# Kernel optimization log

Measured on AMD Instinct MI355X. Metric: run time of the kernel, lower is better.

## Reference

```python
import jax, jax.numpy as jnp
import numpy as np

B, LI, LT = 1, 2048, 256
HID, HEADS, HD = 3072, 24, 128
MLP = 4 * HID  # 12288
EPS = 1e-6


def setup_inputs() -> dict:
    key = jax.random.key(0)
    ks = jax.random.split(key, 12)
    n = lambda k, s, sc=1.0: jax.random.normal(k, s, dtype=jnp.float32) * sc
    # RoPE tables, interleaved-pair layout over head_dim
    theta = 10000.0 ** (-jnp.arange(0, HD, 2, dtype=jnp.float32) / HD)  # [HD/2]
    ang = jnp.arange(LI, dtype=jnp.float32)[:, None] * theta[None, :]   # [LI, HD/2]
    freqs_cos = jnp.repeat(jnp.cos(ang), 2, axis=-1)  # [LI, HD]
    freqs_sin = jnp.repeat(jnp.sin(ang), 2, axis=-1)
    return {
        "img": n(ks[0], (B, LI, HID)),
        "txt": n(ks[1], (B, LT, HID)),
        "vec": n(ks[2], (B, HID)),
        "freqs_cos": freqs_cos,
        "freqs_sin": freqs_sin,
        "w1": n(ks[3], (3 * HID + MLP, HID), 0.02),
        "b1": jnp.zeros((3 * HID + MLP,), jnp.float32),
        "w2": n(ks[4], (HID, HID + MLP), 0.02),
        "b2": jnp.zeros((HID,), jnp.float32),
        "q_norm_w": jnp.ones((HD,), jnp.float32),
        "k_norm_w": jnp.ones((HD,), jnp.float32),
        "mod_w": n(ks[5], (3 * HID, HID), 0.02),
        "mod_b": jnp.zeros((3 * HID,), jnp.float32),
        "txt_len": LT,
    }


def _layernorm(x):  # no affine, eps=1e-6
    mu = x.mean(-1, keepdims=True)
    var = ((x - mu) ** 2).mean(-1, keepdims=True)
    return (x - mu) * jax.lax.rsqrt(var + EPS)


def _rmsnorm(x, w):  # per-head-dim RMSNorm with affine weight
    ms = (x * x).mean(-1, keepdims=True)
    return x * jax.lax.rsqrt(ms + EPS) * w


def _rope(x, cos, sin):  # x: [B,L,H,D]; interleaved complex rotation
    xr = x.reshape(*x.shape[:-1], HD // 2, 2)
    rot = jnp.stack([-xr[..., 1], xr[..., 0]], axis=-1).reshape(x.shape)
    return x * cos[None, :, None, :] + rot * sin[None, :, None, :]


def reference(img, txt, vec, freqs_cos, freqs_sin, w1, b1, w2, b2,
              q_norm_w, k_norm_w, mod_w, mod_b, txt_len):
    H = img.shape[-1]
    Li = img.shape[1]
    # modulation: SiLU(vec) @ W -> shift, scale, gate
    mod = jax.nn.silu(vec) @ mod_w.T + mod_b           # [B, 3H]
    shift, scale, gate = jnp.split(mod, 3, axis=-1)
    modulate = lambda x: x * (1.0 + scale[:, None, :]) + shift[:, None, :]
    img_mod = modulate(_layernorm(img))
    txt_mod = modulate(_layernorm(txt))
    x_mod = jnp.concatenate([img_mod, txt_mod], axis=1)  # [B,S,H]
    Bb, S = x_mod.shape[0], x_mod.shape[1]
    # fused QKV projection (slices of linear1)
    qkv = x_mod @ w1[: 3 * H].T + b1[: 3 * H]
    q, k, v = [t.reshape(Bb, S, HEADS, HD) for t in jnp.split(qkv, 3, axis=-1)]
    q = _rmsnorm(q, q_norm_w)
    k = _rmsnorm(k, k_norm_w)
    # RoPE only on the img portion of the sequence
    q = jnp.concatenate([_rope(q[:, :Li], freqs_cos, freqs_sin), q[:, Li:]], axis=1)
    k = jnp.concatenate([_rope(k[:, :Li], freqs_cos, freqs_sin), k[:, Li:]], axis=1)
    # full (non-causal) attention over img+txt tokens
    logits = jnp.einsum('bqhd,bkhd->bhqk', q, k) * (HD ** -0.5)
    probs = jax.nn.softmax(logits, axis=-1)
    attn = jnp.einsum('bhqk,bkhd->bqhd', probs, v).reshape(Bb, S, H)
    # MLP branch (linear1 mlp slice) with gelu-tanh, then fused linear2
    mlp = jax.nn.gelu(x_mod @ w1[3 * H:].T + b1[3 * H:], approximate=True)
    out = jnp.concatenate([attn, mlp], axis=-1) @ w2.T + b2  # [B,S,H]
    img_out = img + gate[:, None, :] * out[:, :-txt_len]
    txt_out = txt + gate[:, None, :] * out[:, -txt_len:]
    return img_out, txt_out
```

## Files before the change

### kernel.cpp

```cpp
#include <hip/hip_runtime.h>
#include <hip/hip_bf16.h>

#define DI __device__ __forceinline__

typedef __attribute__((ext_vector_type(8))) short bf8;
typedef __attribute__((ext_vector_type(4))) float f4;
typedef __attribute__((ext_vector_type(8))) unsigned short us8;

#define LI    2048
#define LT    256
#define SEQ   2304
#define HID   3072
#define NHEAD 24
#define HD    128
#define N1    21504
#define QKVW  9216
#define N2CAT 15360

DI unsigned short f2bf(float f) {
  union { float f; unsigned u; } v; v.f = f;
  unsigned r = v.u + 0x7FFFu + ((v.u >> 16) & 1u);
  return (unsigned short)(r >> 16);
}
DI float bf2f(unsigned short h) {
  union { unsigned u; float f; } v; v.u = ((unsigned)h) << 16;
  return v.f;
}

DI void gload16(const void* g, void* l) {
  __builtin_amdgcn_global_load_lds(
      (const __attribute__((address_space(1))) void*)g,
      (__attribute__((address_space(3))) void*)l, 16, 0, 0);
}

DI f4 mfma16(bf8 a, bf8 b, f4 c) {
  return __builtin_amdgcn_mfma_f32_16x16x32_bf16(a, b, c, 0, 0, 0);
}

__global__ void k_mod(const float* __restrict__ vec, const float* __restrict__ mw,
                      const float* __restrict__ mb, float* __restrict__ mod) {
  int row = blockIdx.x * 4 + (threadIdx.x >> 6);
  int lane = threadIdx.x & 63;
  const float4* wr = (const float4*)(mw + (size_t)row * HID);
  const float4* vv = (const float4*)vec;
  float s = 0.f;
  for (int i = lane; i < HID / 4; i += 64) {
    float4 w4 = wr[i], x4 = vv[i];
    s += (x4.x / (1.f + __expf(-x4.x))) * w4.x;
    s += (x4.y / (1.f + __expf(-x4.y))) * w4.y;
    s += (x4.z / (1.f + __expf(-x4.z))) * w4.z;
    s += (x4.w / (1.f + __expf(-x4.w))) * w4.w;
  }
#pragma unroll
  for (int m = 32; m; m >>= 1) s += __shfl_xor(s, m);
  if (lane == 0) mod[row] = s + mb[row];
}

__global__ void k_lnmod(const float* __restrict__ img, const float* __restrict__ txt,
                        const float* __restrict__ mod, unsigned short* __restrict__ xmod) {
  int t = blockIdx.x;
  const float* x = (t < LI) ? (img + (size_t)t * HID) : (txt + (size_t)(t - LI) * HID);
  const float4* x4 = (const float4*)x;
  float4 v[3];
  float s = 0.f, ss = 0.f;
#pragma unroll
  for (int j = 0; j < 3; ++j) {
    v[j] = x4[threadIdx.x + j * 256];
    s  += v[j].x + v[j].y + v[j].z + v[j].w;
    ss += v[j].x * v[j].x + v[j].y * v[j].y + v[j].z * v[j].z + v[j].w * v[j].w;
  }
#pragma unroll
  for (int m = 32; m; m >>= 1) { s += __shfl_xor(s, m); ss += __shfl_xor(ss, m); }
  __shared__ float red[8];
  int wv = threadIdx.x >> 6;
  if ((threadIdx.x & 63) == 0) { red[wv] = s; red[4 + wv] = ss; }
  __syncthreads();
  s = red[0] + red[1] + red[2] + red[3];
  ss = red[4] + red[5] + red[6] + red[7];
  float mu = s * (1.f / HID);
  float var = ss * (1.f / HID) - mu * mu;
  float inv = rsqrtf(var + 1e-6f);
  const float* shift = mod;
  const float* scale = mod + HID;
#pragma unroll
  for (int j = 0; j < 3; ++j) {
    int i = threadIdx.x + j * 256;
    int c = i * 4;
    ushort4 o;
    o.x = f2bf((v[j].x - mu) * inv * (1.f + scale[c + 0]) + shift[c + 0]);
    o.y = f2bf((v[j].y - mu) * inv * (1.f + scale[c + 1]) + shift[c + 1]);
    o.z = f2bf((v[j].z - mu) * inv * (1.f + scale[c + 2]) + shift[c + 2]);
    o.w = f2bf((v[j].w - mu) * inv * (1.f + scale[c + 3]) + shift[c + 3]);
    ((ushort4*)xmod)[(size_t)t * (HID / 4) + i] = o;
  }
}

__global__ void k_f2bf(const float* __restrict__ in, unsigned short* __restrict__ out, int n4) {
  int stride = gridDim.x * blockDim.x;
  for (int i = blockIdx.x * blockDim.x + threadIdx.x; i < n4; i += stride) {
    float4 f = ((const float4*)in)[i];
    ushort4 o;
    o.x = f2bf(f.x); o.y = f2bf(f.y); o.z = f2bf(f.z); o.w = f2bf(f.w);
    ((ushort4*)out)[i] = o;
  }
}

#define BAR()    asm volatile("s_barrier" ::: "memory")
#define VMCNT6() asm volatile("s_waitcnt vmcnt(6)" ::: "memory")
#define VMCNT2() asm volatile("s_waitcnt vmcnt(2)" ::: "memory")
#define VMCNT0() asm volatile("s_waitcnt vmcnt(0)" ::: "memory")
#define LGKM0()  do { asm volatile("s_waitcnt lgkmcnt(0)" ::: "memory"); \
                      __builtin_amdgcn_sched_barrier(0); } while (0)

__global__ __launch_bounds__(512, 2) void k_gemm1(const unsigned short* __restrict__ xmod,
    const unsigned short* __restrict__ w1b, const float* __restrict__ b1,
    unsigned short* __restrict__ qkv, unsigned short* __restrict__ amlp) {
  __shared__ unsigned short As[2][256 * 64];
  __shared__ unsigned short Bs[2][256 * 64];
  const int K = HID;
  const int NT = K / 64;
  int tid = threadIdx.x, lane = tid & 63, wid = tid >> 6;
  int wr = wid >> 2, wc = wid & 3;

  int b = blockIdx.x;
  const int Q = 756 / 8, R = 756 % 8;
  int xcd = b & 7, idx = b >> 3;
  int wg = (xcd < R ? xcd * (Q + 1) : R * (Q + 1) + (xcd - R) * Q) + idx;
  int bm = wg % 9, bn = wg / 9;

  const unsigned short* Ag = xmod + (size_t)bm * 256 * K;
  const unsigned short* Bg = w1b + (size_t)bn * 256 * K;

  int sgran = (lane & 7) ^ ((lane >> 3) & 7);
  int srow = wid * 16 + (lane >> 3);

#define STAGE_A(bufi, t, hh) do { \
    gload16(Ag + (size_t)((hh)*128 + srow) * K + (t)*64 + sgran*8, \
            &As[bufi][((hh)*128 + wid*16) * 64]); \
    gload16(Ag + (size_t)((hh)*128 + 8 + srow) * K + (t)*64 + sgran*8, \
            &As[bufi][((hh)*128 + wid*16 + 8) * 64]); \
  } while (0)
#define STAGE_B(bufi, t, hh) do { \
    gload16(Bg + (size_t)((hh)*128 + srow) * K + (t)*64 + sgran*8, \
            &Bs[bufi][((hh)*128 + wid*16) * 64]); \
    gload16(Bg + (size_t)((hh)*128 + 8 + srow) * K + (t)*64 + sgran*8, \
            &Bs[bufi][((hh)*128 + wid*16 + 8) * 64]); \
  } while (0)

  int rA = wr * 128 + (lane & 15);
  int rB = wc * 64 + (lane & 15);
  int qq = lane >> 4, l7 = lane & 7;

  f4 acc[8][4];
#pragma unroll
  for (int m = 0; m < 8; ++m)
#pragma unroll
    for (int n = 0; n < 4; ++n) acc[m][n] = (f4){0.f, 0.f, 0.f, 0.f};
  bf8 aL[4][2], aH[4][2], bL[2][2], bH[2][2];

#define RD(buf, r, s) (*(const bf8*)&buf[(r) * 64 + ((((s)*4 + qq) ^ l7) << 3)])

#define GROUP(C, tn, tn2) do { \
     \
    _Pragma("unroll") for (int m = 0; m < 4; ++m) \
      _Pragma("unroll") for (int s = 0; s < 2; ++s) aL[m][s] = RD(As[C], rA + m*16, s); \
    _Pragma("unroll") for (int n = 0; n < 2; ++n) \
      _Pragma("unroll") for (int s = 0; s < 2; ++s) bL[n][s] = RD(Bs[C], rB + n*16, s); \
    STAGE_A(1-(C), tn, 1); STAGE_B(1-(C), tn, 0); STAGE_B(1-(C), tn, 1); \
    LGKM0(); \
    __builtin_amdgcn_s_setprio(1); \
    _Pragma("unroll") for (int m = 0; m < 4; ++m) \
      _Pragma("unroll") for (int n = 0; n < 2; ++n) \
        _Pragma("unroll") for (int s = 0; s < 2; ++s) \
          acc[m][n] = mfma16(aL[m][s], bL[n][s], acc[m][n]); \
    __builtin_amdgcn_s_setprio(0); \
     \
    _Pragma("unroll") for (int n = 0; n < 2; ++n) \
      _Pragma("unroll") for (int s = 0; s < 2; ++s) bH[n][s] = RD(Bs[C], rB + (n+2)*16, s); \
    LGKM0(); \
    __builtin_amdgcn_s_setprio(1); \
    _Pragma("unroll") for (int m = 0; m < 4; ++m) \
      _Pragma("unroll") for (int n = 0; n < 2; ++n) \
        _Pragma("unroll") for (int s = 0; s < 2; ++s) \
          acc[m][n+2] = mfma16(aL[m][s], bH[n][s], acc[m][n+2]); \
    __builtin_amdgcn_s_setprio(0); \
     \
    _Pragma("unroll") for (int m = 0; m < 4; ++m) \
      _Pragma("unroll") for (int s = 0; s < 2; ++s) aH[m][s] = RD(As[C], rA + (m+4)*16, s); \
    LGKM0(); \
    BAR(); \
    __builtin_amdgcn_s_setprio(1); \
    _Pragma("unroll") for (int m = 0; m < 4; ++m) \
      _Pragma("unroll") for (int n = 0; n < 2; ++n) \
        _Pragma("unroll") for (int s = 0; s < 2; ++s) \
          acc[m+4][n+2] = mfma16(aH[m][s], bH[n][s], acc[m+4][n+2]); \
    __builtin_amdgcn_s_setprio(0); \
     \
    STAGE_A(C, tn2, 0); \
    __builtin_amdgcn_s_setprio(1); \
    _Pragma("unroll") for (int m = 0; m < 4; ++m) \
      _Pragma("unroll") for (int n = 0; n < 2; ++n) \
        _Pragma("unroll") for (int s = 0; s < 2; ++s) \
          acc[m+4][n] = mfma16(aH[m][s], bL[n][s], acc[m+4][n]); \
    __builtin_amdgcn_s_setprio(0); \
    VMCNT2(); \
    BAR(); \
  } while (0)

  STAGE_A(0, 0, 0); STAGE_A(0, 0, 1); STAGE_B(0, 0, 0); STAGE_B(0, 0, 1);
  STAGE_A(1, 1, 0);
  VMCNT2();
  BAR();

  for (int i = 0; i < NT / 2; ++i) {
    int t0 = 2 * i;
    int n1 = t0 + 2; if (n1 > NT - 1) n1 = NT - 1;
    int n2 = t0 + 3; if (n2 > NT - 1) n2 = NT - 1;
    GROUP(0, t0 + 1, n1);
    GROUP(1, n1, n2);
  }
  VMCNT0();

  int r0 = bm * 256 + wr * 128 + ((lane >> 4) << 2);
  int c0 = bn * 256 + wc * 64 + (lane & 15);
  bool isqkv = (bn * 256) < QKVW;
#pragma unroll
  for (int m = 0; m < 8; ++m) {
#pragma unroll
    for (int n = 0; n < 4; ++n) {
      int col = c0 + n * 16;
      float bias = b1[col];
#pragma unroll
      for (int j = 0; j < 4; ++j) {
        int row = r0 + m * 16 + j;
        float v = acc[m][n][j] + bias;
        if (isqkv) {
          qkv[(size_t)row * QKVW + col] = f2bf(v);
        } else {
          float u = 0.7978845608f * (v + 0.044715f * v * v * v);
          float g = v / (1.f + __expf(-2.f * u));
          amlp[(size_t)row * N2CAT + (col - 6144)] = f2bf(g);
        }
      }
    }
  }
#undef STAGE_A
#undef STAGE_B
#undef RD
#undef GROUP
}

__global__ __launch_bounds__(512, 2) void k_gemm2(const unsigned short* __restrict__ amlp,
    const unsigned short* __restrict__ w2b, const float* __restrict__ b2,
    const float* __restrict__ img, const float* __restrict__ txt,
    const float* __restrict__ gate, float* __restrict__ out) {
  __shared__ unsigned short As[3][256 * 64];
  __shared__ unsigned short Bs[3][128 * 64];
  const int K = N2CAT;
  const int NT = K / 64;
  int tid = threadIdx.x, lane = tid & 63, wid = tid >> 6;
  int wr = wid >> 1, wc = wid & 1;

  int b = blockIdx.x;
  int bsw = (b & 7) * 27 + (b >> 3);
  int bm = bsw % 9, bn = bsw / 9;

  const unsigned short* Ag = amlp + (size_t)bm * 256 * K;
  const unsigned short* Bg = w2b + (size_t)bn * 128 * K;

  int sgran = (lane & 7) ^ ((lane >> 3) & 7);
  int srow = wid * 16 + (lane >> 3);

#define STAGE2_A(bufi, t, hh) do { \
    gload16(Ag + (size_t)((hh)*128 + srow) * K + (t)*64 + sgran*8, \
            &As[bufi][((hh)*128 + wid*16) * 64]); \
    gload16(Ag + (size_t)((hh)*128 + 8 + srow) * K + (t)*64 + sgran*8, \
            &As[bufi][((hh)*128 + wid*16 + 8) * 64]); \
  } while (0)
#define STAGE2_B(bufi, t) do { \
    gload16(Bg + (size_t)(srow) * K + (t)*64 + sgran*8, \
            &Bs[bufi][(wid*16) * 64]); \
    gload16(Bg + (size_t)(8 + srow) * K + (t)*64 + sgran*8, \
            &Bs[bufi][(wid*16 + 8) * 64]); \
  } while (0)

  int rA = wr * 64 + (lane & 15);
  int rB = wc * 64 + (lane & 15);
  int qq = lane >> 4, l7 = lane & 7;

  f4 acc[4][4];
#pragma unroll
  for (int m = 0; m < 4; ++m)
#pragma unroll
    for (int n = 0; n < 4; ++n) acc[m][n] = (f4){0.f, 0.f, 0.f, 0.f};
  bf8 aL[2][2], aH[2][2], bL[2][2], bH[2][2];

#define RD2(buf, r, s) (*(const bf8*)&buf[(r) * 64 + ((((s)*4 + qq) ^ l7) << 3)])

#define GROUP2(C, SB, t, full) do { \
     \
    _Pragma("unroll") for (int m = 0; m < 2; ++m) \
      _Pragma("unroll") for (int s = 0; s < 2; ++s) aL[m][s] = RD2(As[C], rA + m*16, s); \
    _Pragma("unroll") for (int n = 0; n < 2; ++n) \
      _Pragma("unroll") for (int s = 0; s < 2; ++s) bL[n][s] = RD2(Bs[C], rB + n*16, s); \
    if (full) STAGE2_A(SB, (t) + 2, 0); \
    LGKM0(); \
    __builtin_amdgcn_s_setprio(1); \
    _Pragma("unroll") for (int m = 0; m < 2; ++m) \
      _Pragma("unroll") for (int n = 0; n < 2; ++n) \
        _Pragma("unroll") for (int s = 0; s < 2; ++s) \
          acc[m][n] = mfma16(aL[m][s], bL[n][s], acc[m][n]); \
    __builtin_amdgcn_s_setprio(0); \
    BAR(); \
     \
    _Pragma("unroll") for (int n = 0; n < 2; ++n) \
      _Pragma("unroll") for (int s = 0; s < 2; ++s) bH[n][s] = RD2(Bs[C], rB + (n+2)*16, s); \
    if (full) STAGE2_A(SB, (t) + 2, 1); \
    LGKM0(); \
    __builtin_amdgcn_s_setprio(1); \
    _Pragma("unroll") for (int m = 0; m < 2; ++m) \
      _Pragma("unroll") for (int n = 0; n < 2; ++n) \
        _Pragma("unroll") for (int s = 0; s < 2; ++s) \
          acc[m][n+2] = mfma16(aL[m][s], bH[n][s], acc[m][n+2]); \
    __builtin_amdgcn_s_setprio(0); \
    BAR(); \
     \
    _Pragma("unroll") for (int m = 0; m < 2; ++m) \
      _Pragma("unroll") for (int s = 0; s < 2; ++s) aH[m][s] = RD2(As[C], rA + (m+2)*16, s); \
    if (full) STAGE2_B(SB, (t) + 2); \
    LGKM0(); \
    __builtin_amdgcn_s_setprio(1); \
    _Pragma("unroll") for (int m = 0; m < 2; ++m) \
      _Pragma("unroll") for (int n = 0; n < 2; ++n) \
        _Pragma("unroll") for (int s = 0; s < 2; ++s) \
          acc[m+2][n+2] = mfma16(aH[m][s], bH[n][s], acc[m+2][n+2]); \
    __builtin_amdgcn_s_setprio(0); \
    BAR(); \
     \
    __builtin_amdgcn_s_setprio(1); \
    _Pragma("unroll") for (int m = 0; m < 2; ++m) \
      _Pragma("unroll") for (int n = 0; n < 2; ++n) \
        _Pragma("unroll") for (int s = 0; s < 2; ++s) \
          acc[m+2][n] = mfma16(aH[m][s], bL[n][s], acc[m+2][n]); \
    __builtin_amdgcn_s_setprio(0); \
    if (full) { VMCNT6(); } else { VMCNT0(); } \
    BAR(); \
  } while (0)

  STAGE2_A(0, 0, 0); STAGE2_A(0, 0, 1); STAGE2_B(0, 0);
  STAGE2_A(1, 1, 0); STAGE2_A(1, 1, 1); STAGE2_B(1, 1);
  VMCNT6();
  BAR();

  for (int i = 0; i < NT / 3; ++i) {
    int t = 3 * i;
    GROUP2(0, 2, t,     (t + 2) < NT);
    GROUP2(1, 0, t + 1, (t + 3) < NT);
    GROUP2(2, 1, t + 2, (t + 4) < NT);
  }
  VMCNT0();

  int r0 = bm * 256 + wr * 64 + ((lane >> 4) << 2);
  int c0 = bn * 128 + wc * 64 + (lane & 15);
#pragma unroll
  for (int m = 0; m < 4; ++m) {
#pragma unroll
    for (int n = 0; n < 4; ++n) {
      int col = c0 + n * 16;
      float bias = b2[col];
      float gt = gate[col];
#pragma unroll
      for (int j = 0; j < 4; ++j) {
        int row = r0 + m * 16 + j;
        float v = acc[m][n][j] + bias;
        float res = (row < LI) ? img[(size_t)row * HID + col]
                               : txt[(size_t)(row - LI) * HID + col];
        out[(size_t)row * HID + col] = res + gt * v;
      }
    }
  }
#undef STAGE2_A
#undef STAGE2_B
#undef RD2
#undef GROUP2
}

__global__ void k_qknorm(unsigned short* __restrict__ qkv, const float* __restrict__ qw,
                         const float* __restrict__ kw, const float* __restrict__ fcos,
                         const float* __restrict__ fsin) {
  int gw = (blockIdx.x * 256 + threadIdx.x) >> 6;
  int lane = threadIdx.x & 63;
  int token = gw / NHEAD, head = gw - token * NHEAD;
  bool dorope = token < LI;
  float c = 1.f, sn = 0.f;
  if (dorope) { c = fcos[token * HD + 2 * lane]; sn = fsin[token * HD + 2 * lane]; }
#pragma unroll
  for (int qk = 0; qk < 2; ++qk) {
    unsigned short* p = qkv + (size_t)token * QKVW + qk * HID + head * HD;
    unsigned u = ((const unsigned*)p)[lane];
    float x0 = bf2f((unsigned short)(u & 0xffff));
    float x1 = bf2f((unsigned short)(u >> 16));
    float ss = x0 * x0 + x1 * x1;
#pragma unroll
    for (int m2 = 32; m2; m2 >>= 1) ss += __shfl_xor(ss, m2);
    float inv = rsqrtf(ss * (1.f / HD) + 1e-6f);
    const float* w = qk ? kw : qw;
    float y0 = x0 * inv * w[2 * lane];
    float y1 = x1 * inv * w[2 * lane + 1];
    if (dorope) { float r0 = y0 * c - y1 * sn; float r1 = y1 * c + y0 * sn; y0 = r0; y1 = r1; }
    ((unsigned*)p)[lane] = ((unsigned)f2bf(y0)) | (((unsigned)f2bf(y1)) << 16);
  }
}

__global__ void k_vt(const unsigned short* __restrict__ qkv, unsigned short* __restrict__ vt) {
  int b = blockIdx.x;
  int h = b / 72; int rem = b - h * 72; int tt = rem >> 1; int dd = rem & 1;
  int t0 = tt * 64, d0 = dd * 64;
  __shared__ unsigned short tile[64 * 65];
  int tid = threadIdx.x;
#pragma unroll
  for (int j = 0; j < 2; ++j) {
    int idx = j * 256 + tid;
    int row = idx >> 3, s = idx & 7;
    us8 vv = *(const us8*)(qkv + (size_t)(t0 + row) * QKVW + 2 * HID + h * HD + d0 + s * 8);
#pragma unroll
    for (int i = 0; i < 8; ++i) tile[row * 65 + s * 8 + i] = vv[i];
  }
  __syncthreads();
#pragma unroll
  for (int j = 0; j < 2; ++j) {
    int idx = j * 256 + tid;
    int dr = idx >> 3, sl = idx & 7;
    us8 o;
#pragma unroll
    for (int i = 0; i < 8; ++i) o[i] = tile[(sl * 8 + i) * 65 + dr];
    *(us8*)(vt + (size_t)(h * HD + d0 + dr) * SEQ + t0 + sl * 8) = o;
  }
}

__global__ __launch_bounds__(256) void k_attn(const unsigned short* __restrict__ qkv,
                                              const unsigned short* __restrict__ vt,
                                              unsigned short* __restrict__ amlp) {
  int b = blockIdx.x;
  int bsw = (b & 7) * 108 + (b >> 3);
  int head = bsw / 36, qt = bsw - head * 36;
  int tid = threadIdx.x, lane = tid & 63, wv = tid >> 6;
  __shared__ unsigned short Qs[64 * 128], Ks[64 * 128], Vs[128 * 64], Ps[64 * 64];
  int qbase = qt * 64;

  {
    int row = tid >> 4, sl = tid & 15;
    int slg = sl ^ (row & 7);
    const unsigned short* qg = qkv + (size_t)(qbase + row) * QKVW + head * HD + slg * 8;
#pragma unroll
    for (int j = 0; j < 4; ++j)
      gload16(qg + (size_t)(j * 16) * QKVW, &Qs[(j * 256 + tid) * 8]);
  }

  float mrun[4], lrun[4];
  f4 oacc[8];
#pragma unroll
  for (int j = 0; j < 4; ++j) { mrun[j] = -1e30f; lrun[j] = 0.f; }
#pragma unroll
  for (int n = 0; n < 8; ++n) oacc[n] = (f4){0.f, 0.f, 0.f, 0.f};
  bf8 qf[4];

  for (int kt = 0; kt < SEQ / 64; ++kt) {
    __syncthreads();
    {
      int rloc = tid >> 4, sl = tid & 15, slg = sl ^ (rloc & 7);
      const unsigned short* kg =
          qkv + HID + (size_t)(kt * 64 + rloc) * QKVW + head * HD + slg * 8;
#pragma unroll
      for (int j = 0; j < 4; ++j) gload16(kg + (size_t)(j * 16) * QKVW, &Ks[(j * 256 + tid) * 8]);
    }
    {
      int rloc = tid >> 3, sl = tid & 7, slg = sl ^ (rloc & 7);
      const unsigned short* vg = vt + (size_t)(head * HD + rloc) * SEQ + kt * 64 + slg * 8;
#pragma unroll
      for (int j = 0; j < 4; ++j) gload16(vg + (size_t)(j * 32) * SEQ, &Vs[(j * 256 + tid) * 8]);
    }
    __syncthreads();
    if (kt == 0) {
#pragma unroll
      for (int kk = 0; kk < 4; ++kk) {
        int row = wv * 16 + (lane & 15);
        int col = (kk * 32 + ((lane >> 4) * 8)) ^ ((lane & 7) << 3);
        qf[kk] = *(const bf8*)&Qs[row * 128 + col];
      }
    }
    f4 sacc[4];
#pragma unroll
    for (int n = 0; n < 4; ++n) sacc[n] = (f4){0.f, 0.f, 0.f, 0.f};
#pragma unroll
    for (int kk = 0; kk < 4; ++kk) {
#pragma unroll
      for (int n = 0; n < 4; ++n) {
        int row = n * 16 + (lane & 15);
        int col = (kk * 32 + ((lane >> 4) * 8)) ^ ((lane & 7) << 3);
        bf8 kf = *(const bf8*)&Ks[row * 128 + col];
        sacc[n] = mfma16(qf[kk], kf, sacc[n]);
      }
    }
    const float SC = 0.08838834764831845f;
    float mj[4];
#pragma unroll
    for (int j = 0; j < 4; ++j)
      mj[j] = fmaxf(fmaxf(sacc[0][j], sacc[1][j]), fmaxf(sacc[2][j], sacc[3][j]));
#pragma unroll
    for (int j = 0; j < 4; ++j) {
#pragma unroll
      for (int mk = 8; mk; mk >>= 1) mj[j] = fmaxf(mj[j], __shfl_xor(mj[j], mk));
    }
    float resc[4], psum[4];
#pragma unroll
    for (int j = 0; j < 4; ++j) {
      float nm = fmaxf(mrun[j], mj[j] * SC);
      resc[j] = __expf(mrun[j] - nm);
      mrun[j] = nm;
      psum[j] = 0.f;
    }
#pragma unroll
    for (int n = 0; n < 4; ++n) {
#pragma unroll
      for (int j = 0; j < 4; ++j) {
        float p = __expf(sacc[n][j] * SC - mrun[j]);
        psum[j] += p;
        int row = wv * 16 + ((lane >> 4) << 2) + j;
        int col = (n * 16 + (lane & 15)) ^ ((row & 7) << 3);
        Ps[row * 64 + col] = f2bf(p);
      }
    }
#pragma unroll
    for (int j = 0; j < 4; ++j) {
#pragma unroll
      for (int mk = 8; mk; mk >>= 1) psum[j] += __shfl_xor(psum[j], mk);
      lrun[j] = lrun[j] * resc[j] + psum[j];
    }
#pragma unroll
    for (int n = 0; n < 8; ++n) {
#pragma unroll
      for (int j = 0; j < 4; ++j) oacc[n][j] *= resc[j];
    }
#pragma unroll
    for (int kk = 0; kk < 2; ++kk) {
      int prow = wv * 16 + (lane & 15);
      int pcol = (kk * 32 + ((lane >> 4) * 8)) ^ ((lane & 7) << 3);
      bf8 pa = *(const bf8*)&Ps[prow * 64 + pcol];
#pragma unroll
      for (int n = 0; n < 8; ++n) {
        int vrow = n * 16 + (lane & 15);
        int vcol = (kk * 32 + ((lane >> 4) * 8)) ^ ((vrow & 7) << 3);
        bf8 vf = *(const bf8*)&Vs[vrow * 64 + vcol];
        oacc[n] = mfma16(pa, vf, oacc[n]);
      }
    }
  }
#pragma unroll
  for (int j = 0; j < 4; ++j) {
    float invl = 1.f / lrun[j];
    int row = qbase + wv * 16 + ((lane >> 4) << 2) + j;
#pragma unroll
    for (int n = 0; n < 8; ++n) {
      int col = head * HD + n * 16 + (lane & 15);
      amlp[(size_t)row * N2CAT + col] = f2bf(oacc[n][j] * invl);
    }
  }
}

extern "C" void kernel_launch(void* const* d_in, const int* in_sizes, int n_in,
                              void* d_out, int out_size, void* d_ws, size_t ws_size,
                              hipStream_t stream) {
  (void)in_sizes; (void)n_in; (void)out_size; (void)ws_size;
  const float* img  = (const float*)d_in[0];
  const float* txt  = (const float*)d_in[1];
  const float* vec  = (const float*)d_in[2];
  const float* fcos = (const float*)d_in[3];
  const float* fsin = (const float*)d_in[4];
  const float* w1   = (const float*)d_in[5];
  const float* b1   = (const float*)d_in[6];
  const float* w2   = (const float*)d_in[7];
  const float* b2   = (const float*)d_in[8];
  const float* qnw  = (const float*)d_in[9];
  const float* knw  = (const float*)d_in[10];
  const float* mw   = (const float*)d_in[11];
  const float* mb   = (const float*)d_in[12];
  float* out = (float*)d_out;

  char* ws = (char*)d_ws;
  float*          mod  = (float*)(ws);
  unsigned short* xmod = (unsigned short*)(ws + 40960);
  unsigned short* w1b  = (unsigned short*)(ws + 14196736);
  unsigned short* qkv  = (unsigned short*)(ws + 146317312);
  unsigned short* amlp = (unsigned short*)(ws + 188784640);
  unsigned short* vtb  = xmod;
  unsigned short* w2b  = w1b;

  k_mod<<<QKVW / 4, 256, 0, stream>>>(vec, mw, mb, mod);
  k_lnmod<<<SEQ, 256, 0, stream>>>(img, txt, mod, xmod);
  k_f2bf<<<2048, 256, 0, stream>>>(w1, w1b, N1 * HID / 4);
  k_gemm1<<<756, 512, 0, stream>>>(xmod, w1b, b1, qkv, amlp);
  k_qknorm<<<SEQ * NHEAD / 4, 256, 0, stream>>>(qkv, qnw, knw, fcos, fsin);
  k_vt<<<NHEAD * 36 * 2, 256, 0, stream>>>(qkv, vtb);
  k_f2bf<<<2048, 256, 0, stream>>>(w2, w2b, HID * N2CAT / 4);
  k_attn<<<864, 256, 0, stream>>>(qkv, vtb, amlp);
  k_gemm2<<<216, 512, 0, stream>>>(amlp, w2b, b2, img, txt, mod + 2 * HID, out);
}
```

Measured before the change: 963.8 us.

## Double-buffer attention K/V loads and fuse side kernels into shared launches

Merges the q/k norm+RoPE kernel and the V-transpose kernel into one launch, split by block index. Folds the w2 fp32-to-bf16 conversion into extra blocks of the attention launch so it runs alongside attention. The attention loop now double-buffers K and V tiles in shared memory, prefetching tile kt+2 while computing on tile kt, which replaces the two full syncthreads per iteration. This cuts launch overhead and hides global-load latency, at the cost of more shared memory per block (and possibly lower occupancy) and conversion blocks contending with attention for bandwidth.

Measured after the change: 909.3 us. 5.7% less time.

```diff
diff --git a/kernel.cpp b/kernel.cpp
--- a/kernel.cpp
+++ b/kernel.cpp
@@ -106,6 +106,7 @@
 }
 
 #define BAR()    asm volatile("s_barrier" ::: "memory")
+#define VMCNT8() asm volatile("s_waitcnt vmcnt(8)" ::: "memory")
 #define VMCNT6() asm volatile("s_waitcnt vmcnt(6)" ::: "memory")
 #define VMCNT2() asm volatile("s_waitcnt vmcnt(2)" ::: "memory")
 #define VMCNT0() asm volatile("s_waitcnt vmcnt(0)" ::: "memory")
@@ -161,7 +162,6 @@
 #define RD(buf, r, s) (*(const bf8*)&buf[(r) * 64 + ((((s)*4 + qq) ^ l7) << 3)])
 
 #define GROUP(C, tn, tn2) do { \
-     \
     _Pragma("unroll") for (int m = 0; m < 4; ++m) \
       _Pragma("unroll") for (int s = 0; s < 2; ++s) aL[m][s] = RD(As[C], rA + m*16, s); \
     _Pragma("unroll") for (int n = 0; n < 2; ++n) \
@@ -174,7 +174,6 @@
         _Pragma("unroll") for (int s = 0; s < 2; ++s) \
           acc[m][n] = mfma16(aL[m][s], bL[n][s], acc[m][n]); \
     __builtin_amdgcn_s_setprio(0); \
-     \
     _Pragma("unroll") for (int n = 0; n < 2; ++n) \
       _Pragma("unroll") for (int s = 0; s < 2; ++s) bH[n][s] = RD(Bs[C], rB + (n+2)*16, s); \
     LGKM0(); \
@@ -184,7 +183,6 @@
         _Pragma("unroll") for (int s = 0; s < 2; ++s) \
           acc[m][n+2] = mfma16(aL[m][s], bH[n][s], acc[m][n+2]); \
     __builtin_amdgcn_s_setprio(0); \
-     \
     _Pragma("unroll") for (int m = 0; m < 4; ++m) \
       _Pragma("unroll") for (int s = 0; s < 2; ++s) aH[m][s] = RD(As[C], rA + (m+4)*16, s); \
     LGKM0(); \
@@ -195,7 +193,6 @@
         _Pragma("unroll") for (int s = 0; s < 2; ++s) \
           acc[m+4][n+2] = mfma16(aH[m][s], bH[n][s], acc[m+4][n+2]); \
     __builtin_amdgcn_s_setprio(0); \
-     \
     STAGE_A(C, tn2, 0); \
     __builtin_amdgcn_s_setprio(1); \
     _Pragma("unroll") for (int m = 0; m < 4; ++m) \
@@ -298,7 +295,6 @@
 #define RD2(buf, r, s) (*(const bf8*)&buf[(r) * 64 + ((((s)*4 + qq) ^ l7) << 3)])
 
 #define GROUP2(C, SB, t, full) do { \
-     \
     _Pragma("unroll") for (int m = 0; m < 2; ++m) \
       _Pragma("unroll") for (int s = 0; s < 2; ++s) aL[m][s] = RD2(As[C], rA + m*16, s); \
     _Pragma("unroll") for (int n = 0; n < 2; ++n) \
@@ -312,7 +308,6 @@
           acc[m][n] = mfma16(aL[m][s], bL[n][s], acc[m][n]); \
     __builtin_amdgcn_s_setprio(0); \
     BAR(); \
-     \
     _Pragma("unroll") for (int n = 0; n < 2; ++n) \
       _Pragma("unroll") for (int s = 0; s < 2; ++s) bH[n][s] = RD2(Bs[C], rB + (n+2)*16, s); \
     if (full) STAGE2_A(SB, (t) + 2, 1); \
@@ -324,7 +319,6 @@
           acc[m][n+2] = mfma16(aL[m][s], bH[n][s], acc[m][n+2]); \
     __builtin_amdgcn_s_setprio(0); \
     BAR(); \
-     \
     _Pragma("unroll") for (int m = 0; m < 2; ++m) \
       _Pragma("unroll") for (int s = 0; s < 2; ++s) aH[m][s] = RD2(As[C], rA + (m+2)*16, s); \
     if (full) STAGE2_B(SB, (t) + 2); \
@@ -336,7 +330,6 @@
           acc[m+2][n+2] = mfma16(aH[m][s], bH[n][s], acc[m+2][n+2]); \
     __builtin_amdgcn_s_setprio(0); \
     BAR(); \
-     \
     __builtin_amdgcn_s_setprio(1); \
     _Pragma("unroll") for (int m = 0; m < 2; ++m) \
       _Pragma("unroll") for (int n = 0; n < 2; ++n) \
@@ -385,68 +378,101 @@
 #undef GROUP2
 }
 
-__global__ void k_qknorm(unsigned short* __restrict__ qkv, const float* __restrict__ qw,
-                         const float* __restrict__ kw, const float* __restrict__ fcos,
-                         const float* __restrict__ fsin) {
-  int gw = (blockIdx.x * 256 + threadIdx.x) >> 6;
-  int lane = threadIdx.x & 63;
-  int token = gw / NHEAD, head = gw - token * NHEAD;
-  bool dorope = token < LI;
-  float c = 1.f, sn = 0.f;
-  if (dorope) { c = fcos[token * HD + 2 * lane]; sn = fsin[token * HD + 2 * lane]; }
-#pragma unroll
-  for (int qk = 0; qk < 2; ++qk) {
-    unsigned short* p = qkv + (size_t)token * QKVW + qk * HID + head * HD;
-    unsigned u = ((const unsigned*)p)[lane];
-    float x0 = bf2f((unsigned short)(u & 0xffff));
-    float x1 = bf2f((unsigned short)(u >> 16));
-    float ss = x0 * x0 + x1 * x1;
-#pragma unroll
-    for (int m2 = 32; m2; m2 >>= 1) ss += __shfl_xor(ss, m2);
-    float inv = rsqrtf(ss * (1.f / HD) + 1e-6f);
-    const float* w = qk ? kw : qw;
-    float y0 = x0 * inv * w[2 * lane];
-    float y1 = x1 * inv * w[2 * lane + 1];
-    if (dorope) { float r0 = y0 * c - y1 * sn; float r1 = y1 * c + y0 * sn; y0 = r0; y1 = r1; }
-    ((unsigned*)p)[lane] = ((unsigned)f2bf(y0)) | (((unsigned)f2bf(y1)) << 16);
-  }
-}
-
-__global__ void k_vt(const unsigned short* __restrict__ qkv, unsigned short* __restrict__ vt) {
+__global__ void k_qkvt(unsigned short* __restrict__ qkv, const float* __restrict__ qw,
+                       const float* __restrict__ kw, const float* __restrict__ fcos,
+                       const float* __restrict__ fsin, unsigned short* __restrict__ vt) {
   int b = blockIdx.x;
-  int h = b / 72; int rem = b - h * 72; int tt = rem >> 1; int dd = rem & 1;
-  int t0 = tt * 64, d0 = dd * 64;
+  int tid = threadIdx.x;
   __shared__ unsigned short tile[64 * 65];
-  int tid = threadIdx.x;
-#pragma unroll
-  for (int j = 0; j < 2; ++j) {
-    int idx = j * 256 + tid;
-    int row = idx >> 3, s = idx & 7;
-    us8 vv = *(const us8*)(qkv + (size_t)(t0 + row) * QKVW + 2 * HID + h * HD + d0 + s * 8);
-#pragma unroll
-    for (int i = 0; i < 8; ++i) tile[row * 65 + s * 8 + i] = vv[i];
-  }
-  __syncthreads();
-#pragma unroll
-  for (int j = 0; j < 2; ++j) {
-    int idx = j * 256 + tid;
-    int dr = idx >> 3, sl = idx & 7;
-    us8 o;
-#pragma unroll
-    for (int i = 0; i < 8; ++i) o[i] = tile[(sl * 8 + i) * 65 + dr];
-    *(us8*)(vt + (size_t)(h * HD + d0 + dr) * SEQ + t0 + sl * 8) = o;
+  if (b < 13824) {
+    int gw = (b * 256 + tid) >> 6;
+    int lane = tid & 63;
+    int token = gw / NHEAD, head = gw - token * NHEAD;
+    bool dorope = token < LI;
+    float c = 1.f, sn = 0.f;
+    if (dorope) { c = fcos[token * HD + 2 * lane]; sn = fsin[token * HD + 2 * lane]; }
+#pragma unroll
+    for (int qk = 0; qk < 2; ++qk) {
+      unsigned short* p = qkv + (size_t)token * QKVW + qk * HID + head * HD;
+      unsigned u = ((const unsigned*)p)[lane];
+      float x0 = bf2f((unsigned short)(u & 0xffff));
+      float x1 = bf2f((unsigned short)(u >> 16));
+      float ss = x0 * x0 + x1 * x1;
+#pragma unroll
+      for (int m2 = 32; m2; m2 >>= 1) ss += __shfl_xor(ss, m2);
+      float inv = rsqrtf(ss * (1.f / HD) + 1e-6f);
+      const float* w = qk ? kw : qw;
+      float y0 = x0 * inv * w[2 * lane];
+      float y1 = x1 * inv * w[2 * lane + 1];
+      if (dorope) { float r0 = y0 * c - y1 * sn; float r1 = y1 * c + y0 * sn; y0 = r0; y1 = r1; }
+      ((unsigned*)p)[lane] = ((unsigned)f2bf(y0)) | (((unsigned)f2bf(y1)) << 16);
+    }
+  } else {
+    int bb = b - 13824;
+    int h = bb / 72; int rem = bb - h * 72; int tt = rem >> 1; int dd = rem & 1;
+    int t0 = tt * 64, d0 = dd * 64;
+#pragma unroll
+    for (int j = 0; j < 2; ++j) {
+      int idx = j * 256 + tid;
+      int row = idx >> 3, s = idx & 7;
+      us8 vv = *(const us8*)(qkv + (size_t)(t0 + row) * QKVW + 2 * HID + h * HD + d0 + s * 8);
+#pragma unroll
+      for (int i = 0; i < 8; ++i) tile[row * 65 + s * 8 + i] = vv[i];
+    }
+    __syncthreads();
+#pragma unroll
+    for (int j = 0; j < 2; ++j) {
+      int idx = j * 256 + tid;
+      int dr = idx >> 3, sl = idx & 7;
+      us8 o;
+#pragma unroll
+      for (int i = 0; i < 8; ++i) o[i] = tile[(sl * 8 + i) * 65 + dr];
+      *(us8*)(vt + (size_t)(h * HD + d0 + dr) * SEQ + t0 + sl * 8) = o;
+    }
   }
 }
 
 __global__ __launch_bounds__(256) void k_attn(const unsigned short* __restrict__ qkv,
                                               const unsigned short* __restrict__ vt,
-                                              unsigned short* __restrict__ amlp) {
+                                              unsigned short* __restrict__ amlp,
+                                              const float* __restrict__ w2,
+                                              unsigned short* __restrict__ w2b) {
   int b = blockIdx.x;
+  int tid = threadIdx.x;
+  if (b >= 864) {
+    int cb = b - 864;
+    const int n4 = HID * N2CAT / 4;
+    for (int i = cb * 256 + tid; i < n4; i += 768 * 256) {
+      float4 f = ((const float4*)w2)[i];
+      ushort4 o;
+      o.x = f2bf(f.x); o.y = f2bf(f.y); o.z = f2bf(f.z); o.w = f2bf(f.w);
+      ((ushort4*)w2b)[i] = o;
+    }
+    return;
+  }
+  __shared__ unsigned short S[40960];
+  unsigned short* Ks = S;
+  unsigned short* Vs = S + 16384;
+  unsigned short* Qs = S + 32768;
+  unsigned short* Ps = S + 32768;
+
   int bsw = (b & 7) * 108 + (b >> 3);
   int head = bsw / 36, qt = bsw - head * 36;
-  int tid = threadIdx.x, lane = tid & 63, wv = tid >> 6;
-  __shared__ unsigned short Qs[64 * 128], Ks[64 * 128], Vs[128 * 64], Ps[64 * 64];
+  int lane = tid & 63, wv = tid >> 6;
   int qbase = qt * 64;
+
+#define STAGEK(dst, t) do { \
+    int rloc_ = tid >> 4, sl_ = tid & 15, slg_ = sl_ ^ (rloc_ & 7); \
+    const unsigned short* kg_ = qkv + HID + (size_t)((t) * 64 + rloc_) * QKVW + head * HD + slg_ * 8; \
+    _Pragma("unroll") for (int j = 0; j < 4; ++j) \
+      gload16(kg_ + (size_t)(j * 16) * QKVW, &(dst)[(j * 256 + tid) * 8]); \
+  } while (0)
+#define STAGEV(dst, t) do { \
+    int rloc_ = tid >> 3, sl_ = tid & 7, slg_ = sl_ ^ (rloc_ & 7); \
+    const unsigned short* vg_ = vt + (size_t)(head * HD + rloc_) * SEQ + (t) * 64 + slg_ * 8; \
+    _Pragma("unroll") for (int j = 0; j < 4; ++j) \
+      gload16(vg_ + (size_t)(j * 32) * SEQ, &(dst)[(j * 256 + tid) * 8]); \
+  } while (0)
 
   {
     int row = tid >> 4, sl = tid & 15;
@@ -456,6 +482,20 @@
     for (int j = 0; j < 4; ++j)
       gload16(qg + (size_t)(j * 16) * QKVW, &Qs[(j * 256 + tid) * 8]);
   }
+  STAGEK(Ks, 0); STAGEV(Vs, 0);
+  STAGEK(Ks + 8192, 1); STAGEV(Vs + 8192, 1);
+  VMCNT8();
+  BAR();
+
+  bf8 qf[4];
+#pragma unroll
+  for (int kk = 0; kk < 4; ++kk) {
+    int row = wv * 16 + (lane & 15);
+    int col = (kk * 32 + ((lane >> 4) * 8)) ^ ((lane & 7) << 3);
+    qf[kk] = *(const bf8*)&Qs[row * 128 + col];
+  }
+  LGKM0();
+  BAR();
 
   float mrun[4], lrun[4];
   f4 oacc[8];
@@ -463,32 +503,11 @@
   for (int j = 0; j < 4; ++j) { mrun[j] = -1e30f; lrun[j] = 0.f; }
 #pragma unroll
   for (int n = 0; n < 8; ++n) oacc[n] = (f4){0.f, 0.f, 0.f, 0.f};
-  bf8 qf[4];
 
   for (int kt = 0; kt < SEQ / 64; ++kt) {
-    __syncthreads();
-    {
-      int rloc = tid >> 4, sl = tid & 15, slg = sl ^ (rloc & 7);
-      const unsigned short* kg =
-          qkv + HID + (size_t)(kt * 64 + rloc) * QKVW + head * HD + slg * 8;
-#pragma unroll
-      for (int j = 0; j < 4; ++j) gload16(kg + (size_t)(j * 16) * QKVW, &Ks[(j * 256 + tid) * 8]);
-    }
-    {
-      int rloc = tid >> 3, sl = tid & 7, slg = sl ^ (rloc & 7);
-      const unsigned short* vg = vt + (size_t)(head * HD + rloc) * SEQ + kt * 64 + slg * 8;
-#pragma unroll
-      for (int j = 0; j < 4; ++j) gload16(vg + (size_t)(j * 32) * SEQ, &Vs[(j * 256 + tid) * 8]);
-    }
-    __syncthreads();
-    if (kt == 0) {
-#pragma unroll
-      for (int kk = 0; kk < 4; ++kk) {
-        int row = wv * 16 + (lane & 15);
-        int col = (kk * 32 + ((lane >> 4) * 8)) ^ ((lane & 7) << 3);
-        qf[kk] = *(const bf8*)&Qs[row * 128 + col];
-      }
-    }
+    int cur = kt & 1;
+    const unsigned short* Kc = Ks + cur * 8192;
+    const unsigned short* Vc = Vs + cur * 8192;
     f4 sacc[4];
 #pragma unroll
     for (int n = 0; n < 4; ++n) sacc[n] = (f4){0.f, 0.f, 0.f, 0.f};
@@ -498,7 +517,7 @@
       for (int n = 0; n < 4; ++n) {
         int row = n * 16 + (lane & 15);
         int col = (kk * 32 + ((lane >> 4) * 8)) ^ ((lane & 7) << 3);
-        bf8 kf = *(const bf8*)&Ks[row * 128 + col];
+        bf8 kf = *(const bf8*)&Kc[row * 128 + col];
         sacc[n] = mfma16(qf[kk], kf, sacc[n]);
       }
     }
@@ -551,11 +570,23 @@
       for (int n = 0; n < 8; ++n) {
         int vrow = n * 16 + (lane & 15);
         int vcol = (kk * 32 + ((lane >> 4) * 8)) ^ ((vrow & 7) << 3);
-        bf8 vf = *(const bf8*)&Vs[vrow * 64 + vcol];
+        bf8 vf = *(const bf8*)&Vc[vrow * 64 + vcol];
         oacc[n] = mfma16(pa, vf, oacc[n]);
       }
     }
-  }
+    BAR();
+    if (kt + 2 < SEQ / 64) {
+      STAGEK(Ks + cur * 8192, kt + 2);
+      STAGEV(Vs + cur * 8192, kt + 2);
+      VMCNT8();
+    } else {
+      VMCNT0();
+    }
+    BAR();
+  }
+#undef STAGEK
+#undef STAGEV
+
 #pragma unroll
   for (int j = 0; j < 4; ++j) {
     float invl = 1.f / lrun[j];
@@ -600,9 +631,7 @@
   k_lnmod<<<SEQ, 256, 0, stream>>>(img, txt, mod, xmod);
   k_f2bf<<<2048, 256, 0, stream>>>(w1, w1b, N1 * HID / 4);
   k_gemm1<<<756, 512, 0, stream>>>(xmod, w1b, b1, qkv, amlp);
-  k_qknorm<<<SEQ * NHEAD / 4, 256, 0, stream>>>(qkv, qnw, knw, fcos, fsin);
-  k_vt<<<NHEAD * 36 * 2, 256, 0, stream>>>(qkv, vtb);
-  k_f2bf<<<2048, 256, 0, stream>>>(w2, w2b, HID * N2CAT / 4);
-  k_attn<<<864, 256, 0, stream>>>(qkv, vtb, amlp);
+  k_qkvt<<<13824 + 1728, 256, 0, stream>>>(qkv, qnw, knw, fcos, fsin, vtb);
+  k_attn<<<864 + 768, 256, 0, stream>>>(qkv, vtb, amlp, w2, w2b);
   k_gemm2<<<216, 512, 0, stream>>>(amlp, w2b, b2, img, txt, mod + 2 * HID, out);
 }
```
